# Optimization experiments

Hardware: AMD Instinct MI355X
Metric: run time of the kernel (lower is better)

The kernel has to match this reference:

```python
import jax, jax.numpy as jnp
import numpy as np

B, SX, TY = 256, 180, 160
D, DK, DV, H, DFF, V = 512, 64, 64, 8, 2048, 30
EPS = 1e-5


def _ln(x, g, b):
    m = jnp.mean(x, axis=-1, keepdims=True)
    v = jnp.mean(jnp.square(x - m), axis=-1, keepdims=True)
    return (x - m) / jnp.sqrt(v + EPS) * g + b


def _mha(q, kv, wq, wk, wv, pw, pb, masked):
    # per-head projections, vectorized over heads (source loops in Python)
    C = q.shape[-1]  # scale uses d_model (input dim), faithful to source
    Q = jnp.einsum('btd,hdk->bhtk', q, wq)
    K = jnp.einsum('bsd,hdk->bhsk', kv, wk)
    Vv = jnp.einsum('bsd,hdv->bhsv', kv, wv)
    W = jnp.einsum('bhtk,bhsk->bhts', Q, K) / (C ** 0.5)
    if masked:
        T = q.shape[1]
        tri = jnp.tril(jnp.ones((T, T), dtype=bool))
        W = jnp.where(tri, W, -jnp.inf)
    W = jax.nn.softmax(W, axis=-1)  # dropout is identity at rate 0 / eval
    out = jnp.einsum('bhts,bhsv->bthv', W, Vv)
    out = out.reshape(q.shape[0], q.shape[1], -1)  # concat heads -> [B,T,H*DV]
    return out @ pw + pb


def _attn_block(q, kv, wq, wk, wv, pw, pb, g, b, masked):
    res = q + _mha(q, kv, wq, wk, wv, pw, pb, masked)
    return _ln(res, g, b)


def _ff_block(x, w1, b1, w2, b2, g, b):
    h = jax.nn.relu(x @ w1 + b1) @ w2 + b2
    return _ln(x + h, g, b)


def setup_inputs() -> dict:
    key = jax.random.key(0)
    ks = iter(jax.random.split(key, 64))

    def n(shape, s=0.05):
        return jax.random.normal(next(ks), shape, jnp.float32) * s

    inp = {}
    inp['x'] = jax.random.normal(next(ks), (B, SX, 2), jnp.float32)
    inp['targets'] = jax.random.randint(next(ks), (B, TY + 1), 0, V, jnp.int32)
    inp['spec_w'] = n((2, D), 0.5)
    inp['spec_b'] = jnp.zeros((D,), jnp.float32)
    inp['pep_emb'] = n((V, D), 0.5)
    for p in ['enc_at', 'dec_sat', 'dec_cat']:
        inp[p + '_wq'] = n((H, D, DK))
        inp[p + '_wk'] = n((H, D, DK))
        inp[p + '_wv'] = n((H, D, DV))
        inp[p + '_pw'] = n((H * DV, D))
        inp[p + '_pb'] = jnp.zeros((D,), jnp.float32)
        inp[p + '_g'] = jnp.ones((D,), jnp.float32)
        inp[p + '_b'] = jnp.zeros((D,), jnp.float32)
    for p in ['enc_ff', 'dec_ff']:
        inp[p + '_w1'] = n((D, DFF))
        inp[p + '_b1'] = jnp.zeros((DFF,), jnp.float32)
        inp[p + '_w2'] = n((DFF, D))
        inp[p + '_b2'] = jnp.zeros((D,), jnp.float32)
        inp[p + '_g'] = jnp.ones((D,), jnp.float32)
        inp[p + '_b'] = jnp.zeros((D,), jnp.float32)
    inp['ll_w'] = n((D, V))
    inp['ll_b'] = jnp.zeros((V,), jnp.float32)
    return inp


def reference(x, targets, spec_w, spec_b, pep_emb,
              enc_at_wq, enc_at_wk, enc_at_wv, enc_at_pw, enc_at_pb, enc_at_g, enc_at_b,
              dec_sat_wq, dec_sat_wk, dec_sat_wv, dec_sat_pw, dec_sat_pb, dec_sat_g, dec_sat_b,
              dec_cat_wq, dec_cat_wk, dec_cat_wv, dec_cat_pw, dec_cat_pb, dec_cat_g, dec_cat_b,
              enc_ff_w1, enc_ff_b1, enc_ff_w2, enc_ff_b2, enc_ff_g, enc_ff_b,
              dec_ff_w1, dec_ff_b1, dec_ff_w2, dec_ff_b2, dec_ff_g, dec_ff_b,
              ll_w, ll_b):
    tgt = targets[:, :-1]
    xe = x @ spec_w + spec_b                      # spectrum embedding [B,SX,D]
    enc = _attn_block(xe, xe, enc_at_wq, enc_at_wk, enc_at_wv, enc_at_pw, enc_at_pb, enc_at_g, enc_at_b, False)
    enc = _ff_block(enc, enc_ff_w1, enc_ff_b1, enc_ff_w2, enc_ff_b2, enc_ff_g, enc_ff_b)
    de = pep_emb[tgt]                             # peptide embedding [B,TY,D]
    d1 = _attn_block(de, de, dec_sat_wq, dec_sat_wk, dec_sat_wv, dec_sat_pw, dec_sat_pb, dec_sat_g, dec_sat_b, True)
    d2 = _attn_block(d1, enc, dec_cat_wq, dec_cat_wk, dec_cat_wv, dec_cat_pw, dec_cat_pb, dec_cat_g, dec_cat_b, False)
    d3 = _ff_block(d2, dec_ff_w1, dec_ff_b1, dec_ff_w2, dec_ff_b2, dec_ff_g, dec_ff_b)
    return d3 @ ll_w + ll_b                       # logits [B,TY,V]
```

## Files before the change

kernel.cpp:

```cpp
#include <hip/hip_runtime.h>
#include <hip/hip_bf16.h>

typedef __hip_bfloat16 bf16;
typedef __attribute__((ext_vector_type(8))) short short8;
typedef __attribute__((ext_vector_type(4))) float f32x4;

#define BB   256
#define SXX  180
#define TYY  160
#define DD   512
#define DKK  64
#define HH   8
#define DFFF 2048
#define VV   30

#define NE (BB * SXX)
#define ND (BB * TYY)
#define N_IN 40

#ifndef __has_builtin
#define __has_builtin(x) 0
#endif

__global__ void k_detect(const unsigned short* __restrict__ probe, int* __restrict__ flag)
{
    if (threadIdx.x == 0 && blockIdx.x == 0)
        *flag = (probe[0] != 0x3F80) ? 1 : 0;
}

__device__ __forceinline__ float ldin(const void* src, long i, int f32)
{
    return f32 ? ((const float*)src)[i] : __bfloat162float(((const bf16*)src)[i]);
}

struct ImpD { const void* src; bf16* dst; int n; int K; int N; int mode; int blk0; int pad; };
struct ImpT { ImpD d[N_IN]; };

__global__ __launch_bounds__(256) void k_import_all(ImpT t, const int* __restrict__ flag)
{
    const int bid = blockIdx.x;
    int which = 0;
    #pragma unroll
    for (int k = 1; k < N_IN; ++k)
        if (bid >= t.d[k].blk0) which = k;
    ImpD d = t.d[which];
    if (d.mode == 3) return;
    long li = (long)(bid - d.blk0) * 256 + threadIdx.x;
    if (li >= d.n) return;
    int f32 = *flag;
    float v;
    if (d.mode == 0) {
        v = ldin(d.src, li, f32);
    } else if (d.mode == 1) {
        int nrow = (int)(li / d.K);
        int k    = (int)(li - (long)nrow * d.K);
        v = (nrow < d.N) ? ldin(d.src, (long)k * d.N + nrow, f32) : 0.f;
    } else {
        int n1 = (int)(li >> 9), dd = (int)(li & 511);
        v = ldin(d.src, (long)(n1 >> 6) * (DD * DKK) + (long)dd * DKK + (n1 & 63), f32);
    }
    d.dst[li] = __float2bfloat16(v);
}

__global__ __launch_bounds__(256) void k_embed_spec(
    const bf16* __restrict__ x, const bf16* __restrict__ w,
    const bf16* __restrict__ b, bf16* __restrict__ out)
{
    long i = (long)blockIdx.x * 256 + threadIdx.x;
    if (i >= (long)NE * DD) return;
    long tok = i >> 9;
    int  d   = (int)(i & 511);
    float x0 = __bfloat162float(x[tok * 2 + 0]);
    float x1 = __bfloat162float(x[tok * 2 + 1]);
    out[i] = __float2bfloat16(x0 * __bfloat162float(w[d])
                            + x1 * __bfloat162float(w[DD + d])
                            + __bfloat162float(b[d]));
}

__global__ __launch_bounds__(256) void k_gather(
    const int* __restrict__ tg, const bf16* __restrict__ emb, bf16* __restrict__ out)
{
    long tok = blockIdx.x;
    int  b   = (int)(tok / TYY);
    int  t   = (int)(tok - (long)b * TYY);
    int  idx = tg[(long)b * (TYY + 1) + t];
    const bf16* src = emb + (long)idx * DD;
    bf16*       dst = out + tok * DD;
    dst[threadIdx.x]       = src[threadIdx.x];
    dst[threadIdx.x + 256] = src[threadIdx.x + 256];
}

__device__ __forceinline__ void stage16(const bf16* g, bf16* l)
{
#if __has_builtin(__builtin_amdgcn_global_load_lds)
    __builtin_amdgcn_global_load_lds(
        (const __attribute__((address_space(1))) unsigned int*)g,
        (__attribute__((address_space(3))) unsigned int*)l, 16, 0, 0);
#else
    *(short8*)l = *(const short8*)g;
#endif
}

__global__ __launch_bounds__(256, 1) void k_mgemm(
    const bf16* __restrict__ A, const bf16* __restrict__ BT,
    const bf16* __restrict__ bias, const bf16* __restrict__ res,
    void* __restrict__ C,
    int M, int N, int K, int lda, int ldb, int ldc,
    int relu, const int* __restrict__ outf32)
{
    __shared__ __align__(16) bf16 sh[16384];

    const int tid  = threadIdx.x;
    const int lane = tid & 63;
    const int w    = tid >> 6;
    const int m0   = blockIdx.y * 128;
    const int n0   = blockIdx.x * 128;
    const int mw   = (w >> 1) * 64;
    const int nw   = (w & 1) * 64;

    f32x4 acc[4][4];
    #pragma unroll
    for (int i = 0; i < 4; ++i)
        #pragma unroll
        for (int j = 0; j < 4; ++j)
            acc[i][j] = (f32x4){0.f, 0.f, 0.f, 0.f};

    const int  sr = tid >> 2;
    const int  sk = (tid & 3) * 8;
    const bf16* Ag0 = A  + (size_t)(m0 + sr) * lda + sk;
    const bf16* Ag1 = Ag0 + (size_t)64 * lda;
    const bf16* Bg0 = BT + (size_t)(n0 + sr) * ldb + sk;
    const bf16* Bg1 = Bg0 + (size_t)64 * ldb;
    const int lofs = sr * 32 + sk;

    const int lc = lane & 15, lq = lane >> 4;

    stage16(Ag0, sh + lofs);
    stage16(Ag1, sh + 2048 + lofs);
    stage16(Bg0, sh + 4096 + lofs);
    stage16(Bg1, sh + 6144 + lofs);

    for (int k0 = 0; k0 < K; k0 += 32) {
        bf16* cb = sh + ((k0 >> 5) & 1) * 8192;
        __syncthreads();
        if (k0 + 32 < K) {
            bf16* nb = sh + ((~(k0 >> 5)) & 1) * 8192;
            stage16(Ag0 + k0 + 32, nb + lofs);
            stage16(Ag1 + k0 + 32, nb + 2048 + lofs);
            stage16(Bg0 + k0 + 32, nb + 4096 + lofs);
            stage16(Bg1 + k0 + 32, nb + 6144 + lofs);
        }

        short8 af[4], bfr[4];
        #pragma unroll
        for (int i = 0; i < 4; ++i)
            af[i] = *(const short8*)(cb + (mw + i * 16 + lc) * 32 + lq * 8);
        #pragma unroll
        for (int j = 0; j < 4; ++j)
            bfr[j] = *(const short8*)(cb + 4096 + (nw + j * 16 + lc) * 32 + lq * 8);

        #pragma unroll
        for (int i = 0; i < 4; ++i)
            #pragma unroll
            for (int j = 0; j < 4; ++j)
                acc[i][j] = __builtin_amdgcn_mfma_f32_16x16x32_bf16(
                    af[i], bfr[j], acc[i][j], 0, 0, 0);
    }

    const int f32o = (outf32 != nullptr) ? *outf32 : 0;

    if (!f32o && (N & 127) == 0) {
        float bv[4];
        #pragma unroll
        for (int j = 0; j < 4; ++j)
            bv[j] = bias ? __bfloat162float(bias[n0 + nw + j * 16 + lc]) : 0.f;
        bf16* ep = sh;
        #pragma unroll
        for (int i = 0; i < 4; ++i) {
            __syncthreads();
            #pragma unroll
            for (int j = 0; j < 4; ++j)
                #pragma unroll
                for (int r = 0; r < 4; ++r) {
                    float v = acc[i][j][r] + bv[j];
                    if (relu && v < 0.f) v = 0.f;
                    int lr = (w >> 1) * 16 + lq * 4 + r;
                    ep[lr * 136 + nw + j * 16 + lc] = __float2bfloat16(v);
                }
            __syncthreads();
            #pragma unroll
            for (int u = 0; u < 2; ++u) {
                int slot = tid + 256 * u;
                int lr   = slot >> 4;
                int cb2  = (slot & 15) << 3;
                int gm   = m0 + 16 * i + ((lr & 16) ? (48 + lr) : lr);
                int gn   = n0 + cb2;
                short8 val = *(short8*)(ep + lr * 136 + cb2);
                if (res) {
                    short8 rv = *(const short8*)(res + (size_t)gm * ldc + gn);
                    #pragma unroll
                    for (int e = 0; e < 8; ++e) {
                        float s = __bfloat162float(((bf16*)&val)[e])
                                + __bfloat162float(((bf16*)&rv)[e]);
                        ((bf16*)&val)[e] = __float2bfloat16(s);
                    }
                }
                *(short8*)((bf16*)C + (size_t)gm * ldc + gn) = val;
            }
        }
    } else {
        #pragma unroll
        for (int j = 0; j < 4; ++j) {
            int gn = n0 + nw + j * 16 + lc;
            if (gn >= N) continue;
            float bvj = bias ? __bfloat162float(bias[gn]) : 0.f;
            #pragma unroll
            for (int i = 0; i < 4; ++i) {
                int gm = m0 + mw + i * 16 + lq * 4;
                #pragma unroll
                for (int r = 0; r < 4; ++r) {
                    float v = acc[i][j][r] + bvj;
                    if (relu && v < 0.f) v = 0.f;
                    size_t off = (size_t)(gm + r) * ldc + gn;
                    if (res) v += __bfloat162float(res[off]);
                    if (f32o) ((float*)C)[off] = v;
                    else      ((bf16*)C)[off]  = __float2bfloat16(v);
                }
            }
        }
    }
}

__global__ __launch_bounds__(256, 1) void k_fattn(
    const bf16* __restrict__ Q, const bf16* __restrict__ Kc,
    const bf16* __restrict__ Vt, bf16* __restrict__ O,
    int T, int S, int b_off, int causal, int ldv)
{
    __shared__ __align__(16) bf16 Pl[4 * 48 * 72];
    const int bl = blockIdx.x, h = blockIdx.y;
    const int tid = threadIdx.x, lane = tid & 63, w = tid >> 6;
    const int lc = lane & 15, lq = lane >> 4;
    const int wr0 = w * 48;
    const float scl = 0.044194173824159216f;

    short8 Qf[3][2];
    #pragma unroll
    for (int i = 0; i < 3; ++i) {
        int t = wr0 + 16 * i + lc;
        if (t >= T) t = T - 1;
        const bf16* qp = Q + ((size_t)(bl + b_off) * T + t) * DD + h * 64;
        #pragma unroll
        for (int kt = 0; kt < 2; ++kt)
            Qf[i][kt] = *(const short8*)(qp + kt * 32 + lq * 8);
    }

    float mrow[3][4], lrow[3][4];
    f32x4 oacc[3][4];
    #pragma unroll
    for (int i = 0; i < 3; ++i)
        #pragma unroll
        for (int r = 0; r < 4; ++r) { mrow[i][r] = -1e30f; lrow[i][r] = 0.f; }
    #pragma unroll
    for (int i = 0; i < 3; ++i)
        #pragma unroll
        for (int n = 0; n < 4; ++n)
            oacc[i][n] = (f32x4){0.f, 0.f, 0.f, 0.f};

    bf16* pw = Pl + w * 48 * 72;

    for (int c0 = 0; c0 < 192; c0 += 64) {
        if (causal && c0 > wr0 + 47) continue;

        short8 Kf[4][2];
        #pragma unroll
        for (int j = 0; j < 4; ++j) {
            int s = c0 + 16 * j + lc;
            if (s >= S) s = S - 1;
            const bf16* kp = Kc + ((size_t)bl * S + s) * DD + h * 64;
            #pragma unroll
            for (int kt = 0; kt < 2; ++kt)
                Kf[j][kt] = *(const short8*)(kp + kt * 32 + lq * 8);
        }

        f32x4 sa[3][4];
        #pragma unroll
        for (int i = 0; i < 3; ++i)
            #pragma unroll
            for (int j = 0; j < 4; ++j)
                sa[i][j] = (f32x4){0.f, 0.f, 0.f, 0.f};
        #pragma unroll
        for (int i = 0; i < 3; ++i)
            #pragma unroll
            for (int j = 0; j < 4; ++j)
                #pragma unroll
                for (int kt = 0; kt < 2; ++kt)
                    sa[i][j] = __builtin_amdgcn_mfma_f32_16x16x32_bf16(
                        Qf[i][kt], Kf[j][kt], sa[i][j], 0, 0, 0);

        #pragma unroll
        for (int i = 0; i < 3; ++i)
            #pragma unroll
            for (int j = 0; j < 4; ++j) {
                int col = c0 + 16 * j + lc;
                #pragma unroll
                for (int r = 0; r < 4; ++r) {
                    int row = wr0 + 16 * i + lq * 4 + r;
                    float v = sa[i][j][r] * scl;
                    if (col >= S || (causal && col > row)) v = -1e30f;
                    sa[i][j][r] = v;
                }
            }

        float corr[3][4];
        #pragma unroll
        for (int i = 0; i < 3; ++i)
            #pragma unroll
            for (int r = 0; r < 4; ++r) {
                float cm = fmaxf(fmaxf(sa[i][0][r], sa[i][1][r]),
                                 fmaxf(sa[i][2][r], sa[i][3][r]));
                cm = fmaxf(cm, __shfl_xor(cm, 1));
                cm = fmaxf(cm, __shfl_xor(cm, 2));
                cm = fmaxf(cm, __shfl_xor(cm, 4));
                cm = fmaxf(cm, __shfl_xor(cm, 8));
                float mn = fmaxf(mrow[i][r], cm);
                corr[i][r] = __expf(mrow[i][r] - mn);
                mrow[i][r] = mn;
            }
        #pragma unroll
        for (int i = 0; i < 3; ++i)
            #pragma unroll
            for (int j = 0; j < 4; ++j)
                #pragma unroll
                for (int r = 0; r < 4; ++r)
                    sa[i][j][r] = __expf(sa[i][j][r] - mrow[i][r]);
        #pragma unroll
        for (int i = 0; i < 3; ++i)
            #pragma unroll
            for (int r = 0; r < 4; ++r) {
                float sm = sa[i][0][r] + sa[i][1][r] + sa[i][2][r] + sa[i][3][r];
                sm += __shfl_xor(sm, 1);
                sm += __shfl_xor(sm, 2);
                sm += __shfl_xor(sm, 4);
                sm += __shfl_xor(sm, 8);
                lrow[i][r] = lrow[i][r] * corr[i][r] + sm;
            }

        #pragma unroll
        for (int i = 0; i < 3; ++i)
            #pragma unroll
            for (int j = 0; j < 4; ++j)
                #pragma unroll
                for (int r = 0; r < 4; ++r)
                    pw[(16 * i + lq * 4 + r) * 72 + 16 * j + lc] =
                        __float2bfloat16(sa[i][j][r]);

        short8 Pf[3][2], Vf[4][2];
        #pragma unroll
        for (int i = 0; i < 3; ++i)
            #pragma unroll
            for (int kt = 0; kt < 2; ++kt)
                Pf[i][kt] = *(const short8*)(pw + (16 * i + lc) * 72 + kt * 32 + lq * 8);
        #pragma unroll
        for (int n = 0; n < 4; ++n)
            #pragma unroll
            for (int kt = 0; kt < 2; ++kt)
                Vf[n][kt] = *(const short8*)(Vt + (size_t)(h * 64 + 16 * n + lc) * ldv
                                             + (size_t)bl * S + c0 + kt * 32 + lq * 8);

        #pragma unroll
        for (int i = 0; i < 3; ++i)
            #pragma unroll
            for (int n = 0; n < 4; ++n) {
                #pragma unroll
                for (int r = 0; r < 4; ++r)
                    oacc[i][n][r] *= corr[i][r];
                #pragma unroll
                for (int kt = 0; kt < 2; ++kt)
                    oacc[i][n] = __builtin_amdgcn_mfma_f32_16x16x32_bf16(
                        Pf[i][kt], Vf[n][kt], oacc[i][n], 0, 0, 0);
            }
    }

    #pragma unroll
    for (int i = 0; i < 3; ++i)
        #pragma unroll
        for (int r = 0; r < 4; ++r) {
            int t = wr0 + 16 * i + lq * 4 + r;
            if (t >= T) continue;
            float inv = 1.f / lrow[i][r];
            bf16* op = O + ((size_t)(bl + b_off) * T + t) * DD + h * 64;
            #pragma unroll
            for (int n = 0; n < 4; ++n)
                op[16 * n + lc] = __float2bfloat16(oacc[i][n][r] * inv);
        }
}

__global__ __launch_bounds__(256) void k_ln(
    const bf16* __restrict__ in, const bf16* __restrict__ g,
    const bf16* __restrict__ b, bf16* __restrict__ out)
{
    __shared__ float red[256];
    long long base = (long long)blockIdx.x * DD;
    int tid = threadIdx.x;
    float v0 = __bfloat162float(in[base + tid]);
    float v1 = __bfloat162float(in[base + 256 + tid]);

    red[tid] = v0 + v1; __syncthreads();
    for (int st = 128; st > 0; st >>= 1) {
        if (tid < st) red[tid] += red[tid + st];
        __syncthreads();
    }
    float mean = red[0] * (1.f / DD);
    __syncthreads();

    float d0 = v0 - mean, d1 = v1 - mean;
    red[tid] = d0 * d0 + d1 * d1; __syncthreads();
    for (int st = 128; st > 0; st >>= 1) {
        if (tid < st) red[tid] += red[tid + st];
        __syncthreads();
    }
    float rstd = rsqrtf(red[0] * (1.f / DD) + 1e-5f);

    out[base + tid] = __float2bfloat16(d0 * rstd * __bfloat162float(g[tid])
                                       + __bfloat162float(b[tid]));
    out[base + 256 + tid] = __float2bfloat16(d1 * rstd * __bfloat162float(g[tid + 256])
                                             + __bfloat162float(b[tid + 256]));
}

static inline void mgemm(hipStream_t s, const bf16* A, const bf16* BT, const bf16* bias,
                         const bf16* res, void* C, int M, int N, int K,
                         int lda, int ldb, int ldc, int relu, const int* outf32 = nullptr)
{
    dim3 grid((N + 127) / 128, M / 128);
    k_mgemm<<<grid, dim3(256), 0, s>>>(A, BT, bias, res, C, M, N, K, lda, ldb, ldc,
                                       relu, outf32);
}

extern "C" void kernel_launch(void* const* d_in, const int* in_sizes, int n_in,
                              void* d_out, int out_size, void* d_ws, size_t ws_size,
                              hipStream_t stream)
{
    char* base = (char*)d_ws;
    size_t o = 0;
    auto take = [&](size_t bytes) { size_t r = o; o += (bytes + 255) & ~(size_t)255; return r; };

    int* dflag = (int*)(base + take(256));
    k_detect<<<dim3(1), dim3(64), 0, stream>>>((const unsigned short*)d_in[10], dflag);

    ImpT tab;
    int blk = 0;
    const bf16* cv[N_IN];
    auto add_imp = [&](int i, int mode, int K, int N, int n_elems) {
        bf16* dst = (bf16*)(base + take((size_t)n_elems * 2));
        tab.d[i] = ImpD{d_in[i], dst, n_elems, K, N, mode, blk, 0};
        blk += (n_elems + 255) / 256;
        cv[i] = dst;
    };
    for (int i = 0; i < N_IN; ++i) {
        if (i == 1) { tab.d[i] = ImpD{nullptr, nullptr, 0, 0, 0, 3, blk, 0}; cv[i] = nullptr; continue; }
        bool qkv = (i == 5 || i == 6 || i == 7 || i == 12 || i == 13 || i == 14 ||
                    i == 19 || i == 20 || i == 21);
        if (qkv)                        add_imp(i, 2, 0, 0, DD * DD);
        else if (i == 8 || i == 15 || i == 22) add_imp(i, 1, DD, DD, DD * DD);
        else if (i == 26 || i == 32)    add_imp(i, 1, DD, DFFF, DFFF * DD);
        else if (i == 28 || i == 34)    add_imp(i, 1, DFFF, DD, DD * DFFF);
        else if (i == 38)               add_imp(i, 1, DD, VV, 128 * DD);
        else                            add_imp(i, 0, 0, 0, in_sizes[i]);
    }
    k_import_all<<<dim3(blk), dim3(256), 0, stream>>>(tab, dflag);

    const int* targets = (const int*)d_in[1];
    const bf16 *x = cv[0], *spec_w = cv[2], *spec_b = cv[3], *pep_emb = cv[4];
    const bf16 *eat_wq = cv[5],  *eat_wk = cv[6],  *eat_wvT = cv[7],  *eat_pw = cv[8],
               *eat_pb = cv[9],  *eat_g  = cv[10], *eat_b   = cv[11];
    const bf16 *sat_wq = cv[12], *sat_wk = cv[13], *sat_wvT = cv[14], *sat_pw = cv[15],
               *sat_pb = cv[16], *sat_g  = cv[17], *sat_b   = cv[18];
    const bf16 *cat_wq = cv[19], *cat_wk = cv[20], *cat_wvT = cv[21], *cat_pw = cv[22],
               *cat_pb = cv[23], *cat_g  = cv[24], *cat_b   = cv[25];
    const bf16 *eff_w1 = cv[26], *eff_b1 = cv[27], *eff_w2 = cv[28], *eff_b2 = cv[29],
               *eff_g  = cv[30], *eff_b  = cv[31];
    const bf16 *dff_w1 = cv[32], *dff_b1 = cv[33], *dff_w2 = cv[34], *dff_b2 = cv[35],
               *dff_g  = cv[36], *dff_b  = cv[37];
    const bf16 *ll_w = cv[38], *ll_b = cv[39];

    const size_t REG = (size_t)NE * DD * 2;
    bf16* A = (bf16*)(base + take(REG));
    bf16* B = (bf16*)(base + take(REG));
    bf16* C = (bf16*)(base + take(REG));
    bf16* D = (bf16*)(base + take(REG + 4096));
    bf16* D2  = D + (size_t)(NE / 2) * DD;
    bf16* H   = B;

    k_embed_spec<<<dim3((NE * DD + 255) / 256), dim3(256), 0, stream>>>(x, spec_w, spec_b, A);

    mgemm(stream, A, eat_wq, nullptr, nullptr, B, NE, DD, DD, DD, DD, DD, 0);
    for (int hb = 0; hb < 2; ++hb) {
        const bf16* kv = A + (size_t)hb * (NE / 2) * DD;
        mgemm(stream, kv, eat_wk, nullptr, nullptr, D, NE / 2, DD, DD, DD, DD, DD, 0);
        mgemm(stream, eat_wvT, kv, nullptr, nullptr, D2, DD, NE / 2, DD, DD, DD, NE / 2, 0);
        k_fattn<<<dim3(BB / 2, HH), dim3(256), 0, stream>>>(
            B, D, D2, B, SXX, SXX, hb * (BB / 2), 0, NE / 2);
    }
    mgemm(stream, B, eat_pw, eat_pb, A, C, NE, DD, DD, DD, DD, DD, 0);
    k_ln<<<dim3(NE), dim3(256), 0, stream>>>(C, eat_g, eat_b, A);

    {
        const int CH = NE / 2;
        for (int c = 0; c < 2; ++c) {
            const bf16* Ain = A + (size_t)c * CH * DD;
            mgemm(stream, Ain, eff_w1, eff_b1, nullptr, H, CH, DFFF, DD, DD, DD, DFFF, 1);
            mgemm(stream, H, eff_w2, eff_b2, Ain, D + (size_t)c * CH * DD,
                  CH, DD, DFFF, DFFF, DFFF, DD, 0);
        }
        k_ln<<<dim3(NE), dim3(256), 0, stream>>>(D, eff_g, eff_b, D);
    }

    k_gather<<<dim3(ND), dim3(256), 0, stream>>>(targets, pep_emb, A);

    bf16* C2d = C + (size_t)(ND / 2) * DD;
    mgemm(stream, A, sat_wq, nullptr, nullptr, B, ND, DD, DD, DD, DD, DD, 0);
    for (int hb = 0; hb < 2; ++hb) {
        const bf16* kv = A + (size_t)hb * (ND / 2) * DD;
        mgemm(stream, kv, sat_wk, nullptr, nullptr, C, ND / 2, DD, DD, DD, DD, DD, 0);
        mgemm(stream, sat_wvT, kv, nullptr, nullptr, C2d, DD, ND / 2, DD, DD, DD, ND / 2, 0);
        k_fattn<<<dim3(BB / 2, HH), dim3(256), 0, stream>>>(
            B, C, C2d, B, TYY, TYY, hb * (BB / 2), 1, ND / 2);
    }
    mgemm(stream, B, sat_pw, sat_pb, A, C, ND, DD, DD, DD, DD, DD, 0);
    k_ln<<<dim3(ND), dim3(256), 0, stream>>>(C, sat_g, sat_b, A);

    bf16* C2e = C + (size_t)(NE / 2) * DD;
    mgemm(stream, A, cat_wq, nullptr, nullptr, B, ND, DD, DD, DD, DD, DD, 0);
    for (int hb = 0; hb < 2; ++hb) {
        const bf16* kv = D + (size_t)hb * (NE / 2) * DD;
        mgemm(stream, kv, cat_wk, nullptr, nullptr, C, NE / 2, DD, DD, DD, DD, DD, 0);
        mgemm(stream, cat_wvT, kv, nullptr, nullptr, C2e, DD, NE / 2, DD, DD, DD, NE / 2, 0);
        k_fattn<<<dim3(BB / 2, HH), dim3(256), 0, stream>>>(
            B, C, C2e, B, TYY, SXX, hb * (BB / 2), 0, NE / 2);
    }
    mgemm(stream, B, cat_pw, cat_pb, A, C, ND, DD, DD, DD, DD, DD, 0);
    k_ln<<<dim3(ND), dim3(256), 0, stream>>>(C, cat_g, cat_b, A);

    {
        const int CH = ND / 2;
        for (int c = 0; c < 2; ++c) {
            const bf16* Ain = A + (size_t)c * CH * DD;
            mgemm(stream, Ain, dff_w1, dff_b1, nullptr, H, CH, DFFF, DD, DD, DD, DFFF, 1);
            mgemm(stream, H, dff_w2, dff_b2, Ain, D + (size_t)c * CH * DD,
                  CH, DD, DFFF, DFFF, DFFF, DD, 0);
        }
        k_ln<<<dim3(ND), dim3(256), 0, stream>>>(D, dff_g, dff_b, D);
    }

    mgemm(stream, D, ll_w, ll_b, nullptr, d_out, ND, VV, DD, DD, DD, VV, 0, dflag);

    (void)in_sizes; (void)n_in; (void)out_size; (void)ws_size;
}
```

Before: 1.760 ms.

## Give each wave private LDS tiles to drop block barriers in GEMM loop

The GEMM main loop now has each wave stage its own 64-row slices of A and B into a private LDS region, so the per-iteration __syncthreads is replaced by s_waitcnt on the wave's own async loads. It also rotates 16-byte k-chunks by row to avoid LDS bank conflicts on the fragment reads. The cost is that LDS doubles to 64KB and global traffic rises, since each A/B row is loaded by two waves instead of once per block.

```diff
diff --git a/kernel.cpp b/kernel.cpp
--- a/kernel.cpp
+++ b/kernel.cpp
@@ -108,7 +108,7 @@
     int M, int N, int K, int lda, int ldb, int ldc,
     int relu, const int* __restrict__ outf32)
 {
-    __shared__ __align__(16) bf16 sh[16384];
+    __shared__ __align__(16) bf16 sh[32768];
 
     const int tid  = threadIdx.x;
     const int lane = tid & 63;
@@ -125,39 +125,44 @@
         for (int j = 0; j < 4; ++j)
             acc[i][j] = (f32x4){0.f, 0.f, 0.f, 0.f};
 
-    const int  sr = tid >> 2;
-    const int  sk = (tid & 3) * 8;
-    const bf16* Ag0 = A  + (size_t)(m0 + sr) * lda + sk;
-    const bf16* Ag1 = Ag0 + (size_t)64 * lda;
-    const bf16* Bg0 = BT + (size_t)(n0 + sr) * ldb + sk;
-    const bf16* Bg1 = Bg0 + (size_t)64 * ldb;
-    const int lofs = sr * 32 + sk;
+    const int srow = lane >> 2;
+    const int kq   = ((lane & 3) - (srow & 3)) & 3;
+    const bf16* AgW = A  + (size_t)(m0 + mw + srow) * lda + kq * 8;
+    const bf16* BgW = BT + (size_t)(n0 + nw + srow) * ldb + kq * 8;
+    bf16* wbuf0 = sh + w * 4096;
+    const int ldst = lane * 8;
 
     const int lc = lane & 15, lq = lane >> 4;
-
-    stage16(Ag0, sh + lofs);
-    stage16(Ag1, sh + 2048 + lofs);
-    stage16(Bg0, sh + 4096 + lofs);
-    stage16(Bg1, sh + 6144 + lofs);
+    const int rchunk = ((lq + lc) & 3) * 8;
+
+    #pragma unroll
+    for (int j = 0; j < 4; ++j) {
+        stage16(AgW + (size_t)(16 * j) * lda, wbuf0 + j * 512 + ldst);
+        stage16(BgW + (size_t)(16 * j) * ldb, wbuf0 + 2048 + j * 512 + ldst);
+    }
 
     for (int k0 = 0; k0 < K; k0 += 32) {
-        bf16* cb = sh + ((k0 >> 5) & 1) * 8192;
-        __syncthreads();
+        bf16* cb = wbuf0 + ((k0 >> 5) & 1) * 16384;
+
         if (k0 + 32 < K) {
-            bf16* nb = sh + ((~(k0 >> 5)) & 1) * 8192;
-            stage16(Ag0 + k0 + 32, nb + lofs);
-            stage16(Ag1 + k0 + 32, nb + 2048 + lofs);
-            stage16(Bg0 + k0 + 32, nb + 4096 + lofs);
-            stage16(Bg1 + k0 + 32, nb + 6144 + lofs);
+            bf16* nb = wbuf0 + ((~(k0 >> 5)) & 1) * 16384;
+            #pragma unroll
+            for (int j = 0; j < 4; ++j) {
+                stage16(AgW + (size_t)(16 * j) * lda + k0 + 32, nb + j * 512 + ldst);
+                stage16(BgW + (size_t)(16 * j) * ldb + k0 + 32, nb + 2048 + j * 512 + ldst);
+            }
+            asm volatile("s_waitcnt vmcnt(8)" ::: "memory");
+        } else {
+            asm volatile("s_waitcnt vmcnt(0)" ::: "memory");
         }
 
         short8 af[4], bfr[4];
         #pragma unroll
         for (int i = 0; i < 4; ++i)
-            af[i] = *(const short8*)(cb + (mw + i * 16 + lc) * 32 + lq * 8);
+            af[i] = *(const short8*)(cb + (16 * i + lc) * 32 + rchunk);
         #pragma unroll
         for (int j = 0; j < 4; ++j)
-            bfr[j] = *(const short8*)(cb + 4096 + (nw + j * 16 + lc) * 32 + lq * 8);
+            bfr[j] = *(const short8*)(cb + 2048 + (16 * j + lc) * 32 + rchunk);
 
         #pragma unroll
         for (int i = 0; i < 4; ++i)
```

After: 2.079 ms. +18.1%, slower.
